# Kernel tuning notes

Hardware: AMD Instinct MI355X
Metric: run time of the kernel (lower is better)

## Reference

```python
import jax, jax.numpy as jnp
import numpy as np

N = 100000          # nodes
E = 1600000         # edges (avg degree 16)
IN_DIM = 128
OUT_DIM = 128
H = 4               # num_heads
D = OUT_DIM // H    # per-head dim = 32
R = 64              # num relations
NEG_SLOPE = 0.2     # DGL GATConv default


def setup_inputs() -> dict:
    key = jax.random.key(0)
    ks = jax.random.split(key, 9)
    h = jax.random.normal(ks[0], (N, IN_DIM), dtype=jnp.float32)
    src = jax.random.randint(ks[1], (E,), 0, N, dtype=jnp.int32)
    dst = jax.random.randint(ks[2], (E,), 0, N, dtype=jnp.int32)
    rel_types = jax.random.randint(ks[3], (E,), 0, R, dtype=jnp.int32)
    # learned params (GATConv fc weight, attention vectors, bias; relation embedding)
    W = jax.random.normal(ks[4], (H * D, IN_DIM), dtype=jnp.float32) * 0.1
    attn_l = jax.random.normal(ks[5], (H, D), dtype=jnp.float32) * 0.1
    attn_r = jax.random.normal(ks[6], (H, D), dtype=jnp.float32) * 0.1
    bias = jax.random.normal(ks[7], (H * D,), dtype=jnp.float32) * 0.01
    rel_emb = jax.random.normal(ks[8], (R, IN_DIM), dtype=jnp.float32) * 0.1
    return {"h": h, "src": src, "dst": dst, "rel_types": rel_types,
            "W": W, "attn_l": attn_l, "attn_r": attn_r, "bias": bias,
            "rel_emb": rel_emb}


def reference(h, src, dst, rel_types, W, attn_l, attn_r, bias, rel_emb):
    # NOTE: the original module builds edata 'e' = h[src] + rel_emb[rel_types],
    # but DGL's GATConv never reads it, so it does not affect the output.
    # Eval mode: feat_drop / attn_drop disabled (deterministic reference).

    # GATConv: project and split heads. [N, H, D]
    feat = (h @ W.T).reshape(N, H, D)
    # per-node attention logits: a_l^T Wh_i, a_r^T Wh_j  -> [N, H]
    el = (feat * attn_l).sum(-1)
    er = (feat * attn_r).sum(-1)
    # per-edge score e_ij = LeakyReLU(el[src] + er[dst])  -> [E, H]
    e = jax.nn.leaky_relu(el[src] + er[dst], NEG_SLOPE)
    # segment softmax over incoming edges of each destination node
    m = jax.ops.segment_max(e, dst, num_segments=N)           # [N, H]
    a = jnp.exp(e - m[dst])                                    # [E, H]
    denom = jax.ops.segment_sum(a, dst, num_segments=N)       # [N, H]
    alpha = a / denom[dst]                                     # [E, H]
    # weighted scatter-aggregate of source features
    msg = feat[src] * alpha[:, :, None]                        # [E, H, D]
    out = jax.ops.segment_sum(msg, dst, num_segments=N)       # [N, H, D]
    out = out + bias.reshape(1, H, D)
    # mean over heads -> [N, D]
    return out.mean(axis=1)
```

## Files before the change

kernel.cpp:

```cpp
#include <hip/hip_runtime.h>
#include <math.h>

#define NEG_SLOPE 0.2f

static __device__ __forceinline__ float bf2f_lo(unsigned int u) {
    return __uint_as_float(u << 16);
}
static __device__ __forceinline__ float bf2f_hi(unsigned int u) {
    return __uint_as_float(u & 0xffff0000u);
}
static __device__ __forceinline__ unsigned short f2bf(float f) {
    unsigned int u = __float_as_uint(f);
    u += 0x7FFFu + ((u >> 16) & 1u);
    return (unsigned short)(u >> 16);
}

__global__ __launch_bounds__(256, 3) void k_gemm_hist(
    const float* __restrict__ h, const float* __restrict__ W,
    unsigned short* __restrict__ featp, int N,
    const int* __restrict__ dst, int* __restrict__ cnt, int* __restrict__ pos,
    int E, int hist_blocks)
{
    __shared__ unsigned short As[64 * 68];
    __shared__ unsigned short Bs[128 * 64];

    if (blockIdx.x < hist_blocks) {
        int t0 = blockIdx.x * 2048 + threadIdx.x;
#pragma unroll
        for (int q = 0; q < 8; ++q) {
            int e = t0 + q * 256;
            if (e < E) pos[e] = atomicAdd(&cnt[dst[e]], 1);
        }
        return;
    }

    const int tid = threadIdx.x;
    const int rb = (blockIdx.x - hist_blocks) * 64;
    const int tc = tid & 31;
    const int tr = tid >> 5;

    float acc[8][4];
#pragma unroll
    for (int i = 0; i < 8; ++i)
#pragma unroll
        for (int j = 0; j < 4; ++j) acc[i][j] = 0.0f;

    for (int kch = 0; kch < 2; ++kch) {
        if (kch) __syncthreads();
#pragma unroll
        for (int i = 0; i < 4; ++i) {
            int chunk = i * 256 + tid;
            int r = chunk >> 4;
            int kc = (chunk & 15) << 2;
            int row = rb + r;
            float4 v = make_float4(0.f, 0.f, 0.f, 0.f);
            if (row < N) v = *(const float4*)(h + (size_t)row * 128 + kch * 64 + kc);
            ushort4 pk;
            pk.x = f2bf(v.x); pk.y = f2bf(v.y); pk.z = f2bf(v.z); pk.w = f2bf(v.w);
            *(ushort4*)(As + r * 68 + kc) = pk;
        }
#pragma unroll
        for (int i = 0; i < 8; ++i) {
            int chunk = i * 256 + tid;
            int c = chunk >> 4;
            int kc = (chunk & 15) << 2;
            float4 v = *(const float4*)(W + (size_t)c * 128 + kch * 64 + kc);
            ushort4 pk;
            pk.x = f2bf(v.x); pk.y = f2bf(v.y); pk.z = f2bf(v.z); pk.w = f2bf(v.w);
            int slot = (kc >> 2) ^ (c & 15);
            *(ushort4*)(Bs + (c << 6) + (slot << 2)) = pk;
        }
        __syncthreads();

#pragma unroll 4
        for (int k4 = 0; k4 < 64; k4 += 4) {
            float bx[4][4];
#pragma unroll
            for (int j = 0; j < 4; ++j) {
                int c = tc + 32 * j;
                int slot = (k4 >> 2) ^ (c & 15);
                uint2 u = *(const uint2*)(Bs + (c << 6) + (slot << 2));
                bx[j][0] = bf2f_lo(u.x); bx[j][1] = bf2f_hi(u.x);
                bx[j][2] = bf2f_lo(u.y); bx[j][3] = bf2f_hi(u.y);
            }
#pragma unroll
            for (int i = 0; i < 8; ++i) {
                uint2 u = *(const uint2*)(As + (tr * 8 + i) * 68 + k4);
                float a0 = bf2f_lo(u.x), a1 = bf2f_hi(u.x);
                float a2 = bf2f_lo(u.y), a3 = bf2f_hi(u.y);
#pragma unroll
                for (int j = 0; j < 4; ++j)
                    acc[i][j] += a0 * bx[j][0] + a1 * bx[j][1] +
                                 a2 * bx[j][2] + a3 * bx[j][3];
            }
        }
    }
#pragma unroll
    for (int i = 0; i < 8; ++i) {
        int row = rb + tr * 8 + i;
        if (row < N) {
            ushort4 pk;
            pk.x = f2bf(acc[i][0]);
            pk.y = f2bf(acc[i][1]);
            pk.z = f2bf(acc[i][2]);
            pk.w = f2bf(acc[i][3]);
            *(ushort4*)(featp + (size_t)row * 128 + tc * 4) = pk;
        }
    }
}

__global__ void k_scan1(const int* __restrict__ cnt, int* __restrict__ bsum, int N) {
    __shared__ int sd[256];
    int t = threadIdx.x;
    int i = blockIdx.x * 256 + t;
    sd[t] = (i < N) ? cnt[i] : 0;
    __syncthreads();
    for (int s = 128; s > 0; s >>= 1) {
        if (t < s) sd[t] += sd[t + s];
        __syncthreads();
    }
    if (t == 0) bsum[blockIdx.x] = sd[0];
}

__global__ void k_scan2(int* __restrict__ bsum, int nb) {
    __shared__ int sd[1024];
    int t = threadIdx.x;
    sd[t] = (t < nb) ? bsum[t] : 0;
    __syncthreads();
    for (int off = 1; off < 1024; off <<= 1) {
        int add = (t >= off) ? sd[t - off] : 0;
        __syncthreads();
        sd[t] += add;
        __syncthreads();
    }
    if (t < nb) bsum[t] = (t == 0) ? 0 : sd[t - 1];
}

__global__ void k_scan3(const int* __restrict__ cnt, const int* __restrict__ bsum,
                        int* __restrict__ row, int N) {
    __shared__ int sd[256];
    int t = threadIdx.x;
    int i = blockIdx.x * 256 + t;
    int v = (i < N) ? cnt[i] : 0;
    sd[t] = v;
    __syncthreads();
    for (int off = 1; off < 256; off <<= 1) {
        int add = (t >= off) ? sd[t - off] : 0;
        __syncthreads();
        sd[t] += add;
        __syncthreads();
    }
    if (i < N) row[i] = bsum[blockIdx.x] + sd[t] - v;
}

__global__ void k_scatter_elr(const int* __restrict__ src, const int* __restrict__ dst,
                              const int* __restrict__ pos, const int* __restrict__ row,
                              int* __restrict__ esrc, int E, int scat_blocks,
                              const unsigned short* __restrict__ featp,
                              const float* __restrict__ attn_l,
                              const float* __restrict__ attn_r,
                              float* __restrict__ el, float* __restrict__ er, int N) {
    if (blockIdx.x < scat_blocks) {
        int e = blockIdx.x * 512 + threadIdx.x;
        if (e < E) esrc[row[dst[e]] + pos[e]] = src[e];
        e += 256;
        if (e < E) esrc[row[dst[e]] + pos[e]] = src[e];
        return;
    }
    int g = (blockIdx.x - scat_blocks) * 256 + threadIdx.x;
    int node = g >> 5;
    int d = g & 31;
    if (node >= N) return;
    uint2 u = *(const uint2*)(featp + (size_t)node * 128 + d * 4);
    float f0 = bf2f_lo(u.x);
    float f1 = bf2f_hi(u.x);
    float f2 = bf2f_lo(u.y);
    float f3 = bf2f_hi(u.y);
    float pl0 = f0 * attn_l[d],      pr0 = f0 * attn_r[d];
    float pl1 = f1 * attn_l[32 + d], pr1 = f1 * attn_r[32 + d];
    float pl2 = f2 * attn_l[64 + d], pr2 = f2 * attn_r[64 + d];
    float pl3 = f3 * attn_l[96 + d], pr3 = f3 * attn_r[96 + d];
#pragma unroll
    for (int m = 1; m < 32; m <<= 1) {
        pl0 += __shfl_xor(pl0, m); pr0 += __shfl_xor(pr0, m);
        pl1 += __shfl_xor(pl1, m); pr1 += __shfl_xor(pr1, m);
        pl2 += __shfl_xor(pl2, m); pr2 += __shfl_xor(pr2, m);
        pl3 += __shfl_xor(pl3, m); pr3 += __shfl_xor(pr3, m);
    }
    if (d == 0) {
        *(float4*)(el + (size_t)node * 4) = make_float4(pl0, pl1, pl2, pl3);
        *(float4*)(er + (size_t)node * 4) = make_float4(pr0, pr1, pr2, pr3);
    }
}

__global__ __launch_bounds__(256) void k_pull(const int* __restrict__ esrc,
                                              const int* __restrict__ row,
                                              const int* __restrict__ cnt,
                                              const float* __restrict__ el,
                                              const float* __restrict__ er,
                                              const unsigned short* __restrict__ featp,
                                              const float* __restrict__ bias,
                                              float* __restrict__ out, int N) {
    int wave = (int)((blockIdx.x * (size_t)blockDim.x + threadIdx.x) >> 6);
    if (wave >= N) return;
    int lane = threadIdx.x & 63;
    int half = lane >> 5;
    int d = lane & 31;
    int start = row[wave];
    int deg = cnt[wave];
    float4 r4 = *(const float4*)(er + 4 * (size_t)wave);

    float acc0 = 0.f, acc1 = 0.f, acc2 = 0.f, acc3 = 0.f;
    float dn0 = 0.f, dn1 = 0.f, dn2 = 0.f, dn3 = 0.f;

    for (int base = 0; base < deg; base += 64) {
        int m = deg - base;
        if (m > 64) m = 64;
        int s_mine = 0;
        float a0 = 0.f, a1 = 0.f, a2 = 0.f, a3 = 0.f;
        if (lane < m) {
            s_mine = esrc[start + base + lane];
            float4 l4 = *(const float4*)(el + 4 * (size_t)s_mine);
            float v0 = l4.x + r4.x; v0 = v0 > 0.f ? v0 : NEG_SLOPE * v0;
            float v1 = l4.y + r4.y; v1 = v1 > 0.f ? v1 : NEG_SLOPE * v1;
            float v2 = l4.z + r4.z; v2 = v2 > 0.f ? v2 : NEG_SLOPE * v2;
            float v3 = l4.w + r4.w; v3 = v3 > 0.f ? v3 : NEG_SLOPE * v3;
            a0 = __expf(v0); a1 = __expf(v1); a2 = __expf(v2); a3 = __expf(v3);
            dn0 += a0; dn1 += a1; dn2 += a2; dn3 += a3;
        }
        for (int ii = 0; ii < m; ii += 2) {
            int i = ii + half;
            int sj   = __shfl(s_mine, i);
            float b0 = __shfl(a0, i);
            float b1 = __shfl(a1, i);
            float b2 = __shfl(a2, i);
            float b3 = __shfl(a3, i);
            uint2 u = *(const uint2*)(featp + (size_t)sj * 128 + d * 4);
            float f0 = bf2f_lo(u.x);
            float f1 = bf2f_hi(u.x);
            float f2 = bf2f_lo(u.y);
            float f3 = bf2f_hi(u.y);
            acc0 += b0 * f0; acc1 += b1 * f1; acc2 += b2 * f2; acc3 += b3 * f3;
        }
    }
    acc0 += __shfl_xor(acc0, 32); acc1 += __shfl_xor(acc1, 32);
    acc2 += __shfl_xor(acc2, 32); acc3 += __shfl_xor(acc3, 32);
#pragma unroll
    for (int m = 1; m < 64; m <<= 1) {
        dn0 += __shfl_xor(dn0, m); dn1 += __shfl_xor(dn1, m);
        dn2 += __shfl_xor(dn2, m); dn3 += __shfl_xor(dn3, m);
    }
    if (half == 0) {
        float msum = 0.f;
        if (dn0 > 0.f)
            msum = acc0 / dn0 + acc1 / dn1 + acc2 / dn2 + acc3 / dn3;
        float b = 0.25f * (bias[d] + bias[32 + d] + bias[64 + d] + bias[96 + d]);
        out[(size_t)wave * 32 + d] = 0.25f * msum + b;
    }
}

extern "C" void kernel_launch(void* const* d_in, const int* in_sizes, int n_in,
                              void* d_out, int out_size, void* d_ws, size_t ws_size,
                              hipStream_t stream) {
    const float* h      = (const float*)d_in[0];
    const int*   src    = (const int*)d_in[1];
    const int*   dst    = (const int*)d_in[2];
    const float* W      = (const float*)d_in[4];
    const float* attn_l = (const float*)d_in[5];
    const float* attn_r = (const float*)d_in[6];
    const float* bias   = (const float*)d_in[7];
    float* out = (float*)d_out;

    const int N = in_sizes[0] / 128;
    const int E = in_sizes[1];

    float* el = (float*)d_ws;
    float* er = el + (size_t)N * 4;
    unsigned short* featp = (unsigned short*)(er + (size_t)N * 4);
    int* cnt  = (int*)(featp + (size_t)N * 128);
    int* row  = cnt + N;
    int* bsum = row + N;
    int* pos  = bsum + 1024;
    int* esrc = pos + E;
    int nb = (N + 255) / 256;

    hipMemsetAsync(cnt, 0, (size_t)N * 4, stream);

    int hist_blocks = (E + 2047) / 2048;
    int gemm_blocks = (N + 63) / 64;
    k_gemm_hist<<<hist_blocks + gemm_blocks, 256, 0, stream>>>(
        h, W, featp, N, dst, cnt, pos, E, hist_blocks);

    k_scan1<<<nb, 256, 0, stream>>>(cnt, bsum, N);
    k_scan2<<<1, 1024, 0, stream>>>(bsum, nb);
    k_scan3<<<nb, 256, 0, stream>>>(cnt, bsum, row, N);

    int scat_blocks = (E + 511) / 512;
    int elr_blocks = ((size_t)N * 32 + 255) / 256;
    k_scatter_elr<<<scat_blocks + elr_blocks, 256, 0, stream>>>(
        src, dst, pos, row, esrc, E, scat_blocks,
        featp, attn_l, attn_r, el, er, N);

    k_pull<<<((size_t)N * 64 + 255) / 256, 256, 0, stream>>>(esrc, row, cnt, el, er,
                                                             featp, bias, out, N);
}
```

Before: 390.1 us.

## Replace scalar bf16 GEMM with MFMA 16x16x32 matrix-core instructions

Rewrites the node projection GEMM inside the fused gemm/histogram kernel to use bf16 MFMA intrinsics instead of scalar FMA loops. The full K=128 of A and B is staged into LDS at once with an XOR swizzle, and each wave computes a 16x128 output tile. Output columns are permuted into a layout the downstream kernels presumably expect. LDS use grows and the occupancy hint is dropped, and the GEMM is only one part of the whole pipeline, which limits the possible gain.

After: 344.5 us. 11.7% less time.

```diff
diff --git a/kernel.cpp b/kernel.cpp
--- a/kernel.cpp
+++ b/kernel.cpp
@@ -2,6 +2,9 @@
 #include <math.h>
 
 #define NEG_SLOPE 0.2f
+
+typedef short bf16x8 __attribute__((ext_vector_type(8)));
+typedef float f32x4 __attribute__((ext_vector_type(4)));
 
 static __device__ __forceinline__ float bf2f_lo(unsigned int u) {
     return __uint_as_float(u << 16);
@@ -15,14 +18,14 @@
     return (unsigned short)(u >> 16);
 }
 
-__global__ __launch_bounds__(256, 3) void k_gemm_hist(
+__global__ __launch_bounds__(256) void k_gemm_hist(
     const float* __restrict__ h, const float* __restrict__ W,
     unsigned short* __restrict__ featp, int N,
     const int* __restrict__ dst, int* __restrict__ cnt, int* __restrict__ pos,
     int E, int hist_blocks)
 {
-    __shared__ unsigned short As[64 * 68];
-    __shared__ unsigned short Bs[128 * 64];
+    __shared__ unsigned short As[64 * 128];
+    __shared__ unsigned short Bs[128 * 128];
 
     if (blockIdx.x < hist_blocks) {
         int t0 = blockIdx.x * 2048 + threadIdx.x;
@@ -36,75 +39,68 @@
 
     const int tid = threadIdx.x;
     const int rb = (blockIdx.x - hist_blocks) * 64;
-    const int tc = tid & 31;
-    const int tr = tid >> 5;
-
-    float acc[8][4];
-#pragma unroll
-    for (int i = 0; i < 8; ++i)
-#pragma unroll
-        for (int j = 0; j < 4; ++j) acc[i][j] = 0.0f;
-
-    for (int kch = 0; kch < 2; ++kch) {
-        if (kch) __syncthreads();
-#pragma unroll
-        for (int i = 0; i < 4; ++i) {
-            int chunk = i * 256 + tid;
-            int r = chunk >> 4;
-            int kc = (chunk & 15) << 2;
-            int row = rb + r;
-            float4 v = make_float4(0.f, 0.f, 0.f, 0.f);
-            if (row < N) v = *(const float4*)(h + (size_t)row * 128 + kch * 64 + kc);
-            ushort4 pk;
-            pk.x = f2bf(v.x); pk.y = f2bf(v.y); pk.z = f2bf(v.z); pk.w = f2bf(v.w);
-            *(ushort4*)(As + r * 68 + kc) = pk;
-        }
-#pragma unroll
-        for (int i = 0; i < 8; ++i) {
-            int chunk = i * 256 + tid;
-            int c = chunk >> 4;
-            int kc = (chunk & 15) << 2;
-            float4 v = *(const float4*)(W + (size_t)c * 128 + kch * 64 + kc);
-            ushort4 pk;
-            pk.x = f2bf(v.x); pk.y = f2bf(v.y); pk.z = f2bf(v.z); pk.w = f2bf(v.w);
-            int slot = (kc >> 2) ^ (c & 15);
-            *(ushort4*)(Bs + (c << 6) + (slot << 2)) = pk;
-        }
-        __syncthreads();
-
-#pragma unroll 4
-        for (int k4 = 0; k4 < 64; k4 += 4) {
-            float bx[4][4];
-#pragma unroll
-            for (int j = 0; j < 4; ++j) {
-                int c = tc + 32 * j;
-                int slot = (k4 >> 2) ^ (c & 15);
-                uint2 u = *(const uint2*)(Bs + (c << 6) + (slot << 2));
-                bx[j][0] = bf2f_lo(u.x); bx[j][1] = bf2f_hi(u.x);
-                bx[j][2] = bf2f_lo(u.y); bx[j][3] = bf2f_hi(u.y);
-            }
-#pragma unroll
-            for (int i = 0; i < 8; ++i) {
-                uint2 u = *(const uint2*)(As + (tr * 8 + i) * 68 + k4);
-                float a0 = bf2f_lo(u.x), a1 = bf2f_hi(u.x);
-                float a2 = bf2f_lo(u.y), a3 = bf2f_hi(u.y);
-#pragma unroll
-                for (int j = 0; j < 4; ++j)
-                    acc[i][j] += a0 * bx[j][0] + a1 * bx[j][1] +
-                                 a2 * bx[j][2] + a3 * bx[j][3];
-            }
-        }
-    }
+
 #pragma unroll
     for (int i = 0; i < 8; ++i) {
-        int row = rb + tr * 8 + i;
+        int chunk = i * 256 + tid;
+        int r = chunk >> 5;
+        int kc = (chunk & 31) << 2;
+        int row = rb + r;
+        float4 v = make_float4(0.f, 0.f, 0.f, 0.f);
+        if (row < N) v = *(const float4*)(h + (size_t)row * 128 + kc);
+        ushort4 pk;
+        pk.x = f2bf(v.x); pk.y = f2bf(v.y); pk.z = f2bf(v.z); pk.w = f2bf(v.w);
+        int byte = (r << 8) + ((kc << 1) ^ ((r & 7) << 4));
+        *(ushort4*)((char*)As + byte) = pk;
+    }
+#pragma unroll
+    for (int i = 0; i < 16; ++i) {
+        int chunk = i * 256 + tid;
+        int c = chunk >> 5;
+        int kc = (chunk & 31) << 2;
+        float4 v = *(const float4*)(W + (size_t)c * 128 + kc);
+        ushort4 pk;
+        pk.x = f2bf(v.x); pk.y = f2bf(v.y); pk.z = f2bf(v.z); pk.w = f2bf(v.w);
+        int byte = (c << 8) + ((kc << 1) ^ ((c & 7) << 4));
+        *(ushort4*)((char*)Bs + byte) = pk;
+    }
+    __syncthreads();
+
+    const int wave = tid >> 6;
+    const int lane = tid & 63;
+    const int dlo = lane & 15;
+    const int kgrp = lane >> 4;
+    const int arow = (wave << 4) + dlo;
+
+    f32x4 acc[8];
+#pragma unroll
+    for (int t = 0; t < 8; ++t) acc[t] = (f32x4){0.f, 0.f, 0.f, 0.f};
+
+#pragma unroll
+    for (int step = 0; step < 4; ++step) {
+        int k2 = (step << 6) + (kgrp << 4);
+        bf16x8 a = *(const bf16x8*)((const char*)As +
+                    ((arow << 8) + (k2 ^ ((arow & 7) << 4))));
+#pragma unroll
+        for (int t = 0; t < 8; ++t) {
+            int col = (t << 4) + dlo;
+            bf16x8 b = *(const bf16x8*)((const char*)Bs +
+                        ((col << 8) + (k2 ^ ((col & 7) << 4))));
+            acc[t] = __builtin_amdgcn_mfma_f32_16x16x32_bf16(a, b, acc[t], 0, 0, 0);
+        }
+    }
+
+#pragma unroll
+    for (int r = 0; r < 4; ++r) {
+        int row = rb + (wave << 4) + ((lane >> 4) << 2) + r;
         if (row < N) {
-            ushort4 pk;
-            pk.x = f2bf(acc[i][0]);
-            pk.y = f2bf(acc[i][1]);
-            pk.z = f2bf(acc[i][2]);
-            pk.w = f2bf(acc[i][3]);
-            *(ushort4*)(featp + (size_t)row * 128 + tc * 4) = pk;
+            ushort4 plo, phi;
+            plo.x = f2bf(acc[0][r]); plo.y = f2bf(acc[2][r]);
+            plo.z = f2bf(acc[4][r]); plo.w = f2bf(acc[6][r]);
+            phi.x = f2bf(acc[1][r]); phi.y = f2bf(acc[3][r]);
+            phi.z = f2bf(acc[5][r]); phi.w = f2bf(acc[7][r]);
+            *(ushort4*)(featp + (size_t)row * 128 + dlo * 4) = plo;
+            *(ushort4*)(featp + (size_t)row * 128 + (dlo + 16) * 4) = phi;
         }
     }
 }
```
